# Kernel tuning notes

Measured on AMD Instinct MI355X. Metric: run time of the kernel, lower is better.

Reference implementation:

```python
import jax, jax.numpy as jnp
import numpy as np

DIM = 128
N = 16384
N_USERS = 512
SAME_USER_BIAS = 5.0

def setup_inputs() -> dict:
    key = jax.random.key(0)
    kx, ku, kq, kk, kv = jax.random.split(key, 5)
    x = jax.random.normal(kx, (N, DIM), dtype=jnp.float32)
    user_ids = jax.random.randint(ku, (N,), 0, N_USERS, dtype=jnp.int64)
    s = 1.0 / np.sqrt(DIM)
    Wq = jax.random.normal(kq, (DIM, DIM), dtype=jnp.float32) * s
    Wk = jax.random.normal(kk, (DIM, DIM), dtype=jnp.float32) * s
    Wv = jax.random.normal(kv, (DIM, DIM), dtype=jnp.float32) * s
    return {"x": x, "user_ids": user_ids, "Wq": Wq, "Wk": Wk, "Wv": Wv}

def reference(x, user_ids, Wq, Wk, Wv):
    # nn.Linear(dim, dim, bias=False): y = x @ W.T
    Q = x @ Wq.T  # [N, d]
    K = x @ Wk.T
    V = x @ Wv.T
    scale = jnp.asarray(DIM ** 0.5, dtype=x.dtype)
    logits = (Q @ K.T) / scale  # [N, N]
    S = (user_ids[:, None] == user_ids[None, :]).astype(logits.dtype)
    logits = logits + SAME_USER_BIAS * S
    A = jax.nn.softmax(logits, axis=1)
    return A @ V
```

## Files before the change

### kernel.cpp

```cpp
#include <hip/hip_runtime.h>
#include <hip/hip_bf16.h>

#define N_TOK 16384
#define DIM   128
#define JT     64

#define KROW 128
#define VROW 64

using bf16x8 = __attribute__((ext_vector_type(8)))  short;
using f32x4  = __attribute__((ext_vector_type(4)))  float;
using f32x16 = __attribute__((ext_vector_type(16))) float;
using i32x4  = __attribute__((ext_vector_type(4)))  int;

static __device__ __forceinline__ unsigned short f2b(float f) {
    union { __hip_bfloat16 h; unsigned short u; } cv;
    cv.h = __float2bfloat16(f);
    return cv.u;
}

static __device__ __forceinline__ bf16x8 load8f(const float* p) {
    float4 a = *reinterpret_cast<const float4*>(p);
    float4 b = *reinterpret_cast<const float4*>(p + 4);
    bf16x8 r;
    r[0] = (short)f2b(a.x); r[1] = (short)f2b(a.y);
    r[2] = (short)f2b(a.z); r[3] = (short)f2b(a.w);
    r[4] = (short)f2b(b.x); r[5] = (short)f2b(b.y);
    r[6] = (short)f2b(b.z); r[7] = (short)f2b(b.w);
    return r;
}

__global__ __launch_bounds__(256)
void marker_kernel(float* out, float val)
{
    int i = blockIdx.x * 256 + threadIdx.x;
    if (i < N_TOK * DIM) out[i] = val;
}

__global__ __launch_bounds__(256)
void qkv_kernel(const float* __restrict__ x,
                const float* __restrict__ wq,
                const float* __restrict__ wk,
                const float* __restrict__ wv,
                unsigned short* __restrict__ Q,
                unsigned short* __restrict__ K,
                unsigned short* __restrict__ Vt)
{
    const int t = threadIdx.x;
    const int wave = t >> 6, lane = t & 63;
    const int ln = lane & 15, quad = lane >> 4, q8 = quad * 8;
    const int z = blockIdx.y;
    const float* W = (z == 0) ? wq : (z == 1) ? wk : wv;
    const int r0 = blockIdx.x * 64 + wave * 16;

    bf16x8 a[4];
#pragma unroll
    for (int ks = 0; ks < 4; ++ks)
        a[ks] = load8f(&x[(size_t)(r0 + ln) * DIM + ks * 32 + q8]);

    f32x4 acc[8];
#pragma unroll
    for (int nt = 0; nt < 8; ++nt) acc[nt] = f32x4{0.f, 0.f, 0.f, 0.f};

#pragma unroll
    for (int nt = 0; nt < 8; ++nt)
#pragma unroll
        for (int ks = 0; ks < 4; ++ks) {
            bf16x8 b = load8f(&W[(size_t)(nt * 16 + ln) * DIM + ks * 32 + q8]);
            acc[nt] = __builtin_amdgcn_mfma_f32_16x16x32_bf16(a[ks], b, acc[nt], 0, 0, 0);
        }

#pragma unroll
    for (int nt = 0; nt < 8; ++nt) {
        const int col = nt * 16 + ln;
        if (z == 2) {
            ushort4 v4;
            v4.x = f2b(acc[nt][0]); v4.y = f2b(acc[nt][1]);
            v4.z = f2b(acc[nt][2]); v4.w = f2b(acc[nt][3]);
            *reinterpret_cast<ushort4*>(&Vt[(size_t)col * N_TOK + r0 + quad * 4]) = v4;
        } else {
            unsigned short* dst = (z == 0) ? Q : K;
#pragma unroll
            for (int r = 0; r < 4; ++r)
                dst[(size_t)(r0 + quad * 4 + r) * DIM + col] = f2b(acc[nt][r]);
        }
    }
}

__global__ __launch_bounds__(256, 2)
void flash_kernel(const unsigned short* __restrict__ Q,
                  const unsigned short* __restrict__ K,
                  const unsigned short* __restrict__ Vt,
                  const unsigned int* __restrict__ u32,
                  int jspan,
                  float* __restrict__ pO, float* __restrict__ pl,
                  float* __restrict__ out)
{
    __shared__ __align__(16) unsigned short kb[2][JT * KROW];
    __shared__ __align__(16) unsigned short vb[2][DIM * VROW];
    __shared__ __align__(16) int   ub[2][JT];
    __shared__ __align__(16) float lbuf[4][32];

    const int t = threadIdx.x;
    const int wave = t >> 6, lane = t & 63;
    const int q31 = lane & 31, hi = lane >> 5;
    const int r0w = blockIdx.x * 128 + wave * 32;
    const int split = blockIdx.y;
    const int j0 = split * jspan;
    const int j1 = j0 + jspan;

    const float lscale = 1.4426950408889634f * 0.08838834764831845f;
    const float cbias  = 5.0f * 1.4426950408889634f - 16.0f;
    const float cnob   = -16.0f;

    bool i64 = true;
    for (int k = 0; k < 64; ++k) i64 = i64 && (u32[2 * k + 1] == 0u);

    bf16x8 qf[8];
#pragma unroll
    for (int dt = 0; dt < 8; ++dt)
        qf[dt] = *reinterpret_cast<const bf16x8*>(
            &Q[(size_t)(r0w + q31) * DIM + dt * 16 + hi * 8]);

    const int uq = (int)(i64 ? u32[2 * (r0w + q31)] : u32[r0w + q31]);

    f32x16 o[4];
#pragma unroll
    for (int nt = 0; nt < 4; ++nt)
#pragma unroll
        for (int r = 0; r < 16; ++r) o[nt][r] = 0.f;
    float lsum = 0.f;

    {
#pragma unroll
        for (int p = 0; p < 4; ++p) {
            int slot = p * 256 + t;
            int row = slot >> 4, seg = slot & 15;
            int ss = seg ^ (row & 7);
            *reinterpret_cast<uint4*>(&kb[0][row * KROW + ss * 8]) =
                *reinterpret_cast<const uint4*>(&K[(size_t)(j0 + row) * DIM + seg * 8]);
        }
#pragma unroll
        for (int p = 0; p < 4; ++p) {
            int slot = p * 256 + t;
            int row = slot >> 3, seg = slot & 7;
            int ss = seg ^ (row & 7);
            *reinterpret_cast<uint4*>(&vb[0][row * VROW + ss * 8]) =
                *reinterpret_cast<const uint4*>(&Vt[(size_t)row * N_TOK + j0 + seg * 8]);
        }
        if (t < JT) {
            int i = j0 + t;
            ub[0][t] = (int)(i64 ? u32[2 * i] : u32[i]);
        }
    }
    __syncthreads();

    int c = 0;
    for (int j = j0; j < j1; j += JT) {
        int jn = j + JT;
        if (jn >= j1) jn = j0;

        uint4 kreg[4];
#pragma unroll
        for (int p = 0; p < 4; ++p) {
            int slot = p * 256 + t;
            int row = slot >> 4, seg = slot & 15;
            kreg[p] = *reinterpret_cast<const uint4*>(&K[(size_t)(jn + row) * DIM + seg * 8]);
        }
        uint4 vreg[4];
#pragma unroll
        for (int p = 0; p < 4; ++p) {
            int slot = p * 256 + t;
            int row = slot >> 3, seg = slot & 7;
            vreg[p] = *reinterpret_cast<const uint4*>(&Vt[(size_t)row * N_TOK + jn + seg * 8]);
        }
        int ureg = 0;
        if (t < JT) ureg = (int)(i64 ? u32[2 * (jn + t)] : u32[jn + t]);

        f32x16 s0v, s1v;
#pragma unroll
        for (int r = 0; r < 16; ++r) { s0v[r] = 0.f; s1v[r] = 0.f; }
        __builtin_amdgcn_s_setprio(1);
#pragma unroll
        for (int dt = 0; dt < 8; ++dt) {
            int seg = (dt * 2 + hi) ^ (q31 & 7);
            bf16x8 k0 = *reinterpret_cast<const bf16x8*>(&kb[c][q31 * KROW + seg * 8]);
            bf16x8 k1 = *reinterpret_cast<const bf16x8*>(&kb[c][(32 + q31) * KROW + seg * 8]);
            s0v = __builtin_amdgcn_mfma_f32_32x32x16_bf16(k0, qf[dt], s0v, 0, 0, 0);
            s1v = __builtin_amdgcn_mfma_f32_32x32x16_bf16(k1, qf[dt], s1v, 0, 0, 0);
        }
        __builtin_amdgcn_s_setprio(0);

        bf16x8 pa[4];
#pragma unroll
        for (int kv32 = 0; kv32 < 2; ++kv32) {
            i32x4 ukg[4];
#pragma unroll
            for (int g = 0; g < 4; ++g)
                ukg[g] = *reinterpret_cast<const i32x4*>(&ub[c][32 * kv32 + 8 * g + 4 * hi]);

            unsigned int dw[4][2];
#pragma unroll
            for (int g = 0; g < 4; ++g) {
                float p0, p1, p2, p3;
                {
                    float v0 = __builtin_fmaf((kv32 ? s1v : s0v)[4 * g + 0], lscale,
                                              (uq == ukg[g][0]) ? cbias : cnob);
                    float v1 = __builtin_fmaf((kv32 ? s1v : s0v)[4 * g + 1], lscale,
                                              (uq == ukg[g][1]) ? cbias : cnob);
                    float v2 = __builtin_fmaf((kv32 ? s1v : s0v)[4 * g + 2], lscale,
                                              (uq == ukg[g][2]) ? cbias : cnob);
                    float v3 = __builtin_fmaf((kv32 ? s1v : s0v)[4 * g + 3], lscale,
                                              (uq == ukg[g][3]) ? cbias : cnob);
                    p0 = exp2f(v0); p1 = exp2f(v1); p2 = exp2f(v2); p3 = exp2f(v3);
                }
                lsum += (p0 + p1) + (p2 + p3);
                dw[g][0] = (unsigned int)f2b(p0) | ((unsigned int)f2b(p1) << 16);
                dw[g][1] = (unsigned int)f2b(p2) | ((unsigned int)f2b(p3) << 16);
            }

#pragma unroll
            for (int kt = 0; kt < 2; ++kt) {
                unsigned int s0d = hi ? dw[2 * kt][0] : dw[2 * kt + 1][0];
                unsigned int s1d = hi ? dw[2 * kt][1] : dw[2 * kt + 1][1];
                unsigned int r0d = (unsigned int)__shfl_xor((int)s0d, 32, 64);
                unsigned int r1d = (unsigned int)__shfl_xor((int)s1d, 32, 64);
                unsigned int k0d = hi ? dw[2 * kt + 1][0] : dw[2 * kt][0];
                unsigned int k1d = hi ? dw[2 * kt + 1][1] : dw[2 * kt][1];
                union { unsigned int u[4]; bf16x8 v; } pu;
                pu.u[0] = hi ? r0d : k0d;
                pu.u[1] = hi ? r1d : k1d;
                pu.u[2] = hi ? k0d : r0d;
                pu.u[3] = hi ? k1d : r1d;
                pa[kv32 * 2 + kt] = pu.v;
            }
        }

#pragma unroll
        for (int p = 0; p < 4; ++p) {
            int slot = p * 256 + t;
            int row = slot >> 4, seg = slot & 15;
            int ss = seg ^ (row & 7);
            *reinterpret_cast<uint4*>(&kb[c ^ 1][row * KROW + ss * 8]) = kreg[p];
        }
        if (t < JT) ub[c ^ 1][t] = ureg;

        __builtin_amdgcn_s_setprio(1);
#pragma unroll
        for (int nt = 0; nt < 4; ++nt) {
            int row = nt * 32 + q31;
#pragma unroll
            for (int ktg = 0; ktg < 4; ++ktg) {
                int seg = (ktg * 2 + hi) ^ (q31 & 7);
                bf16x8 b = *reinterpret_cast<const bf16x8*>(&vb[c][row * VROW + seg * 8]);
                o[nt] = __builtin_amdgcn_mfma_f32_32x32x16_bf16(pa[ktg], b, o[nt], 0, 0, 0);
            }
        }
        __builtin_amdgcn_s_setprio(0);

#pragma unroll
        for (int p = 0; p < 4; ++p) {
            int slot = p * 256 + t;
            int row = slot >> 3, seg = slot & 7;
            int ss = seg ^ (row & 7);
            *reinterpret_cast<uint4*>(&vb[c ^ 1][row * VROW + ss * 8]) = vreg[p];
        }

        __syncthreads();
        c ^= 1;
    }

    lsum += __shfl_xor(lsum, 32, 64);

    if (out != nullptr) {
        bool lbad = !(lsum > 0.f) || !(lsum < 3.0e38f);
        float inv = 1.0f / lsum;
        if (hi == 0) lbuf[wave][q31] = lbad ? -1.0f : inv;
        __syncthreads();
        f32x4 ivg[4];
#pragma unroll
        for (int g = 0; g < 4; ++g)
            ivg[g] = *reinterpret_cast<const f32x4*>(&lbuf[wave][8 * g + 4 * hi]);
#pragma unroll
        for (int nt = 0; nt < 4; ++nt)
#pragma unroll
            for (int g = 0; g < 4; ++g)
#pragma unroll
                for (int i = 0; i < 4; ++i) {
                    int row = r0w + 8 * g + 4 * hi + i;
                    float iv = ivg[g][i];
                    float v = o[nt][4 * g + i] * iv;
                    if (v != v) v = 12345.0f;
                    if (iv < 0.f) v = 23456.0f;
                    out[(size_t)row * DIM + nt * 32 + q31] = v;
                }
    } else {
        const size_t base = (size_t)split * N_TOK;
        if (hi == 0) pl[base + r0w + q31] = lsum;
#pragma unroll
        for (int nt = 0; nt < 4; ++nt)
#pragma unroll
            for (int g = 0; g < 4; ++g)
#pragma unroll
                for (int i = 0; i < 4; ++i) {
                    int row = r0w + 8 * g + 4 * hi + i;
                    pO[(base + row) * DIM + nt * 32 + q31] = o[nt][4 * g + i];
                }
    }
}

__global__ __launch_bounds__(256)
void merge_kernel(const float* __restrict__ pO, const float* __restrict__ pl,
                  float* __restrict__ out, int ns)
{
    const int t = threadIdx.x;
    const int wave = t >> 6, lane = t & 63;
    const int row = blockIdx.x * 4 + wave;
    const int c = lane * 2;

    float l = 0.f;
    for (int s = 0; s < ns; ++s) l += pl[(size_t)s * N_TOK + row];
    bool lbad = !(l > 0.f) || !(l < 3.0e38f);
    float inv = 1.0f / l;

    float a0 = 0.f, a1 = 0.f;
    for (int s = 0; s < ns; ++s) {
        const float2 v = *reinterpret_cast<const float2*>(
            &pO[((size_t)s * N_TOK + row) * DIM + c]);
        a0 += v.x; a1 += v.y;
    }
    float v0 = a0 * inv, v1 = a1 * inv;
    if (v0 != v0) v0 = 12345.0f;
    if (v1 != v1) v1 = 12345.0f;
    if (lbad) { v0 = 23456.0f; v1 = 23456.0f; }
    float2 res; res.x = v0; res.y = v1;
    *reinterpret_cast<float2*>(&out[(size_t)row * DIM + c]) = res;
}

extern "C" void kernel_launch(void* const* d_in, const int* in_sizes, int n_in,
                              void* d_out, int out_size, void* d_ws, size_t ws_size,
                              hipStream_t stream)
{
    float* out = (float*)d_out;

    bool ok = (n_in == 5) &&
              in_sizes[0] == N_TOK * DIM && in_sizes[1] == N_TOK &&
              in_sizes[2] == DIM * DIM && in_sizes[3] == DIM * DIM &&
              in_sizes[4] == DIM * DIM && out_size == N_TOK * DIM;
    if (!ok) { marker_kernel<<<8192, 256, 0, stream>>>(out, 5555.f); return; }

    const float*        xf  = (const float*)d_in[0];
    const unsigned int* u32 = (const unsigned int*)d_in[1];
    const float*        wqf = (const float*)d_in[2];
    const float*        wkf = (const float*)d_in[3];
    const float*        wvf = (const float*)d_in[4];

    char* ws = (char*)d_ws;
    size_t off = 0;
    unsigned short* Q  = (unsigned short*)(ws + off); off += (size_t)N_TOK * DIM * 2;
    unsigned short* K  = (unsigned short*)(ws + off); off += (size_t)N_TOK * DIM * 2;
    unsigned short* Vt = (unsigned short*)(ws + off); off += (size_t)N_TOK * DIM * 2;

    if (ws_size < off) { marker_kernel<<<8192, 256, 0, stream>>>(out, 4444.f); return; }

    const size_t per_split = (size_t)N_TOK * DIM * 4 + (size_t)N_TOK * 4;
    int nsplit = 1;
    if (ws_size >= off + 4 * per_split)      nsplit = 4;
    else if (ws_size >= off + 2 * per_split) nsplit = 2;

    qkv_kernel<<<dim3(N_TOK / 64, 3), 256, 0, stream>>>(xf, wqf, wkf, wvf, Q, K, Vt);

    if (nsplit >= 2) {
        float* pO = (float*)(ws + off);
        float* pl = (float*)(ws + off + (size_t)nsplit * N_TOK * DIM * 4);
        flash_kernel<<<dim3(N_TOK / 128, nsplit), 256, 0, stream>>>(
            Q, K, Vt, u32, N_TOK / nsplit, pO, pl, nullptr);
        merge_kernel<<<N_TOK / 4, 256, 0, stream>>>(pO, pl, out, nsplit);
    } else {
        flash_kernel<<<dim3(N_TOK / 128, 1), 256, 0, stream>>>(
            Q, K, Vt, u32, N_TOK, nullptr, nullptr, out);
    }
}
```

Before: 291.1 us.

## Halve KV tile to 32, raise occupancy to 4 blocks, allow 8-way split

Shrinks the key/value tile from 64 to 32 tokens, which halves LDS buffers and drops one score accumulator, and reworks the V swizzle and the load/MFMA loops to match. Launch bounds go from 2 to 4 blocks per CU to raise occupancy for latency hiding. The split-K count can now reach 8 when workspace allows, giving more blocks. In exchange each iteration does less work per barrier, so sync and loop overhead grow, and more partial outputs must be merged.

```diff
diff --git a/kernel.cpp b/kernel.cpp
--- a/kernel.cpp
+++ b/kernel.cpp
@@ -3,10 +3,10 @@
 
 #define N_TOK 16384
 #define DIM   128
-#define JT     64
+#define JT     32
 
 #define KROW 128
-#define VROW 64
+#define VROW 32
 
 using bf16x8 = __attribute__((ext_vector_type(8)))  short;
 using f32x4  = __attribute__((ext_vector_type(4)))  float;
@@ -87,7 +87,7 @@
     }
 }
 
-__global__ __launch_bounds__(256, 2)
+__global__ __launch_bounds__(256, 4)
 void flash_kernel(const unsigned short* __restrict__ Q,
                   const unsigned short* __restrict__ K,
                   const unsigned short* __restrict__ Vt,
@@ -133,7 +133,7 @@
 
     {
 #pragma unroll
-        for (int p = 0; p < 4; ++p) {
+        for (int p = 0; p < 2; ++p) {
             int slot = p * 256 + t;
             int row = slot >> 4, seg = slot & 15;
             int ss = seg ^ (row & 7);
@@ -141,10 +141,10 @@
                 *reinterpret_cast<const uint4*>(&K[(size_t)(j0 + row) * DIM + seg * 8]);
         }
 #pragma unroll
-        for (int p = 0; p < 4; ++p) {
-            int slot = p * 256 + t;
-            int row = slot >> 3, seg = slot & 7;
-            int ss = seg ^ (row & 7);
+        for (int p = 0; p < 2; ++p) {
+            int slot = p * 256 + t;
+            int row = slot >> 2, seg = slot & 3;
+            int ss = seg ^ ((row >> 1) & 3);
             *reinterpret_cast<uint4*>(&vb[0][row * VROW + ss * 8]) =
                 *reinterpret_cast<const uint4*>(&Vt[(size_t)row * N_TOK + j0 + seg * 8]);
         }
@@ -160,60 +160,50 @@
         int jn = j + JT;
         if (jn >= j1) jn = j0;
 
-        uint4 kreg[4];
-#pragma unroll
-        for (int p = 0; p < 4; ++p) {
+        uint4 kreg[2];
+#pragma unroll
+        for (int p = 0; p < 2; ++p) {
             int slot = p * 256 + t;
             int row = slot >> 4, seg = slot & 15;
             kreg[p] = *reinterpret_cast<const uint4*>(&K[(size_t)(jn + row) * DIM + seg * 8]);
         }
-        uint4 vreg[4];
-#pragma unroll
-        for (int p = 0; p < 4; ++p) {
-            int slot = p * 256 + t;
-            int row = slot >> 3, seg = slot & 7;
+        uint4 vreg[2];
+#pragma unroll
+        for (int p = 0; p < 2; ++p) {
+            int slot = p * 256 + t;
+            int row = slot >> 2, seg = slot & 3;
             vreg[p] = *reinterpret_cast<const uint4*>(&Vt[(size_t)row * N_TOK + jn + seg * 8]);
         }
         int ureg = 0;
         if (t < JT) ureg = (int)(i64 ? u32[2 * (jn + t)] : u32[jn + t]);
 
-        f32x16 s0v, s1v;
-#pragma unroll
-        for (int r = 0; r < 16; ++r) { s0v[r] = 0.f; s1v[r] = 0.f; }
+        f32x16 sv;
+#pragma unroll
+        for (int r = 0; r < 16; ++r) sv[r] = 0.f;
         __builtin_amdgcn_s_setprio(1);
 #pragma unroll
         for (int dt = 0; dt < 8; ++dt) {
             int seg = (dt * 2 + hi) ^ (q31 & 7);
             bf16x8 k0 = *reinterpret_cast<const bf16x8*>(&kb[c][q31 * KROW + seg * 8]);
-            bf16x8 k1 = *reinterpret_cast<const bf16x8*>(&kb[c][(32 + q31) * KROW + seg * 8]);
-            s0v = __builtin_amdgcn_mfma_f32_32x32x16_bf16(k0, qf[dt], s0v, 0, 0, 0);
-            s1v = __builtin_amdgcn_mfma_f32_32x32x16_bf16(k1, qf[dt], s1v, 0, 0, 0);
+            sv = __builtin_amdgcn_mfma_f32_32x32x16_bf16(k0, qf[dt], sv, 0, 0, 0);
         }
         __builtin_amdgcn_s_setprio(0);
 
-        bf16x8 pa[4];
-#pragma unroll
-        for (int kv32 = 0; kv32 < 2; ++kv32) {
+        bf16x8 pa[2];
+        {
             i32x4 ukg[4];
 #pragma unroll
             for (int g = 0; g < 4; ++g)
-                ukg[g] = *reinterpret_cast<const i32x4*>(&ub[c][32 * kv32 + 8 * g + 4 * hi]);
+                ukg[g] = *reinterpret_cast<const i32x4*>(&ub[c][8 * g + 4 * hi]);
 
             unsigned int dw[4][2];
 #pragma unroll
             for (int g = 0; g < 4; ++g) {
-                float p0, p1, p2, p3;
-                {
-                    float v0 = __builtin_fmaf((kv32 ? s1v : s0v)[4 * g + 0], lscale,
-                                              (uq == ukg[g][0]) ? cbias : cnob);
-                    float v1 = __builtin_fmaf((kv32 ? s1v : s0v)[4 * g + 1], lscale,
-                                              (uq == ukg[g][1]) ? cbias : cnob);
-                    float v2 = __builtin_fmaf((kv32 ? s1v : s0v)[4 * g + 2], lscale,
-                                              (uq == ukg[g][2]) ? cbias : cnob);
-                    float v3 = __builtin_fmaf((kv32 ? s1v : s0v)[4 * g + 3], lscale,
-                                              (uq == ukg[g][3]) ? cbias : cnob);
-                    p0 = exp2f(v0); p1 = exp2f(v1); p2 = exp2f(v2); p3 = exp2f(v3);
-                }
+                float v0 = __builtin_fmaf(sv[4 * g + 0], lscale, (uq == ukg[g][0]) ? cbias : cnob);
+                float v1 = __builtin_fmaf(sv[4 * g + 1], lscale, (uq == ukg[g][1]) ? cbias : cnob);
+                float v2 = __builtin_fmaf(sv[4 * g + 2], lscale, (uq == ukg[g][2]) ? cbias : cnob);
+                float v3 = __builtin_fmaf(sv[4 * g + 3], lscale, (uq == ukg[g][3]) ? cbias : cnob);
+                float p0 = exp2f(v0), p1 = exp2f(v1), p2 = exp2f(v2), p3 = exp2f(v3);
                 lsum += (p0 + p1) + (p2 + p3);
                 dw[g][0] = (unsigned int)f2b(p0) | ((unsigned int)f2b(p1) << 16);
                 dw[g][1] = (unsigned int)f2b(p2) | ((unsigned int)f2b(p3) << 16);
@@ -232,12 +222,12 @@
                 pu.u[1] = hi ? r1d : k1d;
                 pu.u[2] = hi ? k0d : r0d;
                 pu.u[3] = hi ? k1d : r1d;
-                pa[kv32 * 2 + kt] = pu.v;
+                pa[kt] = pu.v;
             }
         }
 
 #pragma unroll
-        for (int p = 0; p < 4; ++p) {
+        for (int p = 0; p < 2; ++p) {
             int slot = p * 256 + t;
             int row = slot >> 4, seg = slot & 15;
             int ss = seg ^ (row & 7);
@@ -250,19 +240,19 @@
         for (int nt = 0; nt < 4; ++nt) {
             int row = nt * 32 + q31;
 #pragma unroll
-            for (int ktg = 0; ktg < 4; ++ktg) {
-                int seg = (ktg * 2 + hi) ^ (q31 & 7);
+            for (int kt = 0; kt < 2; ++kt) {
+                int seg = (kt * 2 + hi) ^ ((row >> 1) & 3);
                 bf16x8 b = *reinterpret_cast<const bf16x8*>(&vb[c][row * VROW + seg * 8]);
-                o[nt] = __builtin_amdgcn_mfma_f32_32x32x16_bf16(pa[ktg], b, o[nt], 0, 0, 0);
+                o[nt] = __builtin_amdgcn_mfma_f32_32x32x16_bf16(pa[kt], b, o[nt], 0, 0, 0);
             }
         }
         __builtin_amdgcn_s_setprio(0);
 
 #pragma unroll
-        for (int p = 0; p < 4; ++p) {
-            int slot = p * 256 + t;
-            int row = slot >> 3, seg = slot & 7;
-            int ss = seg ^ (row & 7);
+        for (int p = 0; p < 2; ++p) {
+            int slot = p * 256 + t;
+            int row = slot >> 2, seg = slot & 3;
+            int ss = seg ^ ((row >> 1) & 3);
             *reinterpret_cast<uint4*>(&vb[c ^ 1][row * VROW + ss * 8]) = vreg[p];
         }
 
@@ -365,7 +355,8 @@
 
     const size_t per_split = (size_t)N_TOK * DIM * 4 + (size_t)N_TOK * 4;
     int nsplit = 1;
-    if (ws_size >= off + 4 * per_split)      nsplit = 4;
+    if (ws_size >= off + 8 * per_split)      nsplit = 8;
+    else if (ws_size >= off + 4 * per_split) nsplit = 4;
     else if (ws_size >= off + 2 * per_split) nsplit = 2;
 
     qkv_kernel<<<dim3(N_TOK / 64, 3), 256, 0, stream>>>(xf, wqf, wkf, wvf, Q, K, Vt);
```

New measurement: 828.0 us. +184.4%, slower.
